# Kernel optimization log

Measured on AMD Instinct MI355X. Metric: run time of the kernel, lower is better.

The kernel has to match this reference:

```python
import jax, jax.numpy as jnp
import numpy as np
from jax import lax

# Quantized ConvBnA block: int8 conv with int32 accumulation, per-channel
# bias add (folded BN), power-of-two requant via arithmetic right shift,
# clamp, and narrow-int cast (uint8 since Act_min >= 0 -> pure_positive).

N, CIN, COUT, H, W, K = 32, 128, 256, 56, 56, 3

def setup_inputs() -> dict:
    key = jax.random.key(0)
    k1, k2, k3 = jax.random.split(key, 3)
    # int8-valued inputs / weights (stored as int32 per harness dtype support)
    x = jax.random.randint(k1, (N, CIN, H, W), -64, 64, dtype=jnp.int32)
    weight = jax.random.randint(k2, (COUT, CIN, K, K), -128, 128, dtype=jnp.int32)
    # BN_shift is negative (shift right by -n = 8 bits)
    n = jnp.full((1, COUT, 1, 1), -8, dtype=jnp.int32)
    # folded-BN integer bias, broadcasts over [N, C, H, W]
    t = jax.random.randint(k3, (1, COUT, 1, 1), -2048, 2048, dtype=jnp.int32)
    act_min = 0
    act_max = 255
    return {"x": x, "weight": weight, "n": n, "t": t,
            "act_min": act_min, "act_max": act_max}

def reference(x, weight, n, t, act_min, act_max):
    # int32-accumulated convolution (stride 1, pad 1, dilation 1, groups 1)
    acc = lax.conv_general_dilated(
        x.astype(jnp.int32), weight.astype(jnp.int32),
        window_strides=(1, 1), padding=((1, 1), (1, 1)),
        dimension_numbers=("NCHW", "OIHW", "NCHW"))
    acc = acc + t                              # folded-BN bias add
    acc = jnp.right_shift(acc, -n)             # pow2 requant, arithmetic shift
    acc = jnp.clip(acc, jnp.int32(act_min), jnp.int32(act_max))
    # pure_positive (Act_min >= 0) -> small unsigned type
    return acc.astype(jnp.uint8)
```

## Files before the change

kernel.cpp:

```cpp
#include <hip/hip_runtime.h>
#include <cstdint>


typedef __attribute__((ext_vector_type(4))) int i32x4;
typedef __attribute__((ext_vector_type(2))) int i32x2;

#define C_IN   128
#define HW2    3136
#define OUT_NSTRIDE 802816

#define XQ_BYTES 12845056
#define WQ_OFF   XQ_BYTES
#define WQ_BYTES 294912
#define ZP_OFF   (WQ_OFF + WQ_BYTES)

__device__ __forceinline__ void gload_lds16(const void* g, void* l) {
  __builtin_amdgcn_global_load_lds(
      (const __attribute__((address_space(1))) void*)(uintptr_t)g,
      (__attribute__((address_space(3))) void*)(uint32_t)(uintptr_t)l,
      16, 0, 0);
}

__global__ __launch_bounds__(256) void prep(const int* __restrict__ x,
                                            const int* __restrict__ w,
                                            char* __restrict__ xq,
                                            char* __restrict__ wq,
                                            int* __restrict__ zp) {
  int bid = blockIdx.x;
  if (bid >= 1568) {
    int id = (bid - 1568) * 256 + threadIdx.x;
    int ci = id & 127;
    int co = (id >> 7) & 255;
    int g  = id >> 15;
    wq[id] = (char)w[co * 1152 + ci * 9 + g];
    if (bid == 1568 && threadIdx.x < 64) zp[threadIdx.x] = 0;
    return;
  }
  int hb = bid % 49;
  int n  = bid / 49;
  int t  = threadIdx.x;
  int cig = t & 15;
  int hw0 = (t >> 4) * 4;
  const int* src = x + n * (C_IN * HW2) + hb * 64 + hw0;
  i32x4 ld[8];
#pragma unroll
  for (int j = 0; j < 8; j++)
    ld[j] = *(const i32x4*)(src + (cig * 8 + j) * HW2);
  char* dst = xq + (size_t)(n * HW2 + hb * 64 + hw0) * 128 + cig * 8;
#pragma unroll
  for (int p = 0; p < 4; p++) {
    unsigned lo = (ld[0][p] & 255) | ((ld[1][p] & 255) << 8) |
                  ((ld[2][p] & 255) << 16) | ((unsigned)(ld[3][p] & 255) << 24);
    unsigned hi = (ld[4][p] & 255) | ((ld[5][p] & 255) << 8) |
                  ((ld[6][p] & 255) << 16) | ((unsigned)(ld[7][p] & 255) << 24);
    i32x2 v; v[0] = (int)lo; v[1] = (int)hi;
    *(i32x2*)(dst + p * 128) = v;
  }
}

__global__ __launch_bounds__(256, 2) void conv_mfma(
    const char* __restrict__ xq, const char* __restrict__ wq,
    const char* __restrict__ zp,
    const int* __restrict__ nshift, const int* __restrict__ tbias,
    const int* __restrict__ aminp, const int* __restrict__ amaxp,
    int* __restrict__ out) {
  __shared__ char lds[65536];

  const int tid = threadIdx.x;
  const int bid = blockIdx.x;
  const int bm = bid & 1;
  const int pb = bid >> 1;
  const int l  = tid & 63;
  const int wid = tid >> 6;
  const int wm = wid >> 1, wn = wid & 1;

  const int chl = tid & 7;
  const int rsw = (tid >> 3) & 7;
  const int chg = chl ^ rsw;
  const int kboff = chg * 16;

  int p_idx[4], p_h[4], p_w[4];
#pragma unroll
  for (int i = 0; i < 4; i++) {
    int pr = (tid >> 3) + i * 32;
    int p  = pb * 128 + pr;
    int n  = p / HW2;
    int hw = p - n * HW2;
    int h  = hw / 56;
    int w  = hw - h * 56;
    p_idx[i] = p; p_h[i] = h; p_w[i] = w;
  }

  auto stageAB = [&](int g, int buf) {
    char* Ab = lds + buf * 32768;
    char* Bb = Ab + 16384;
    const int dh = g / 3 - 1, dw = g % 3 - 1;
    const int doff = dh * 56 + dw;
    const char* wsrc = wq + (((g * 256 + bm * 128)) << 7) + kboff;
#pragma unroll
    for (int i = 0; i < 4; i++) {
      int row = (tid >> 3) + i * 32;
      gload_lds16(wsrc + (row << 7), Ab + (tid + i * 256) * 16);
    }
#pragma unroll
    for (int i = 0; i < 4; i++) {
      int h2 = p_h[i] + dh, w2 = p_w[i] + dw;
      bool valid = ((unsigned)h2 < 56u) && ((unsigned)w2 < 56u);
      const char* gp = valid ? (xq + ((size_t)(p_idx[i] + doff) << 7) + kboff)
                             : zp;
      gload_lds16(gp, Bb + (tid + i * 256) * 16);
    }
  };

  i32x4 acc[4][4] = {};
  const int lrow = l & 15;
  const int lk   = (l >> 4) * 16;
  const int lsw  = (l & 7) << 4;

  auto computeStep = [&](int buf) {
    char* Ab = lds + buf * 32768;
    char* Bb = Ab + 16384;
#pragma unroll
    for (int kk = 0; kk < 2; kk++) {
      i32x4 a[4], b[4];
      const int cb = ((kk * 64 + lk) ^ lsw);
#pragma unroll
      for (int mi = 0; mi < 4; mi++) {
        int row = wm * 64 + mi * 16 + lrow;
        a[mi] = *(const i32x4*)(Ab + (row << 7) + cb);
      }
#pragma unroll
      for (int ni = 0; ni < 4; ni++) {
        int row = wn * 64 + ni * 16 + lrow;
        b[ni] = *(const i32x4*)(Bb + (row << 7) + cb);
      }
#pragma unroll
      for (int mi = 0; mi < 4; mi++)
#pragma unroll
        for (int ni = 0; ni < 4; ni++)
          acc[mi][ni] = __builtin_amdgcn_mfma_i32_16x16x64_i8(
              a[mi], b[ni], acc[mi][ni], 0, 0, 0);
    }
  };

  stageAB(0, 0);
#pragma unroll 1
  for (int s = 0; s < 9; ++s) {
    const int s1 = s + 1;
    if (s1 < 9) stageAB(s1, s1 & 1);
    __builtin_amdgcn_sched_barrier(0);
    if (s1 < 9) { asm volatile("s_waitcnt vmcnt(8)" ::: "memory"); }
    else        { asm volatile("s_waitcnt vmcnt(0)" ::: "memory"); }
    __builtin_amdgcn_s_barrier();
    __builtin_amdgcn_sched_barrier(0);
    computeStep(s & 1);
    __builtin_amdgcn_sched_barrier(0);
    __builtin_amdgcn_s_barrier();
    __builtin_amdgcn_sched_barrier(0);
  }

  const int amin = aminp[0], amax = amaxp[0];
  int pbase[4];
#pragma unroll
  for (int ni = 0; ni < 4; ni++) {
    int pp = pb * 128 + wn * 64 + ni * 16 + lrow;
    int nn = pp / HW2;
    int hh = pp - nn * HW2;
    pbase[ni] = nn * OUT_NSTRIDE + hh;
  }
#pragma unroll
  for (int mi = 0; mi < 4; mi++) {
    int co0 = bm * 128 + wm * 64 + mi * 16 + ((l >> 4) << 2);
    const int4 t4 = *(const int4*)(tbias + co0);
    const int4 n4 = *(const int4*)(nshift + co0);
#pragma unroll
    for (int ni = 0; ni < 4; ni++) {
#pragma unroll
      for (int r = 0; r < 4; r++) {
        int tv = (r == 0) ? t4.x : (r == 1) ? t4.y : (r == 2) ? t4.z : t4.w;
        int nv = (r == 0) ? n4.x : (r == 1) ? n4.y : (r == 2) ? n4.z : n4.w;
        int v = acc[mi][ni][r] + tv;
        v = v >> (-nv);
        v = v < amin ? amin : (v > amax ? amax : v);
        out[pbase[ni] + (co0 + r) * HW2] = v;
      }
    }
  }
}

extern "C" void kernel_launch(void* const* d_in, const int* in_sizes, int n_in,
                              void* d_out, int out_size, void* d_ws, size_t ws_size,
                              hipStream_t stream) {
  const int* x      = (const int*)d_in[0];
  const int* w      = (const int*)d_in[1];
  const int* nshift = (const int*)d_in[2];
  const int* tbias  = (const int*)d_in[3];
  const int* aminp  = (const int*)d_in[4];
  const int* amaxp  = (const int*)d_in[5];
  int* out = (int*)d_out;

  char* xq = (char*)d_ws;
  char* wq = (char*)d_ws + WQ_OFF;
  char* zp = (char*)d_ws + ZP_OFF;

  hipLaunchKernelGGL(prep, dim3(2720), dim3(256), 0, stream, x, w, xq, wq, (int*)zp);
  hipLaunchKernelGGL(conv_mfma, dim3(1568), dim3(256), 0, stream,
                     xq, wq, zp, nshift, tbias, aminp, amaxp, out);
}
```

Baseline: 182.5 us.

## Load weight fragments directly into registers and stage only activations in LDS

Weight tiles no longer go through LDS: each wave reads its A fragments straight from global memory into registers at the start of every filter tap. Only the shifted activation tiles remain double-buffered in LDS, which halves the shared-memory footprint and removes the A-side LDS writes and reads. The wait count is lowered to match the smaller number of outstanding staging loads. MFMA sections are also wrapped in s_setprio to favour waves that are issuing matrix ops. The trade-off is that weight loads are neither prefetched nor shared across waves, so their global or L2 latency sits on the critical path each step and sibling waves read the same data twice.

```diff
diff --git a/kernel.cpp b/kernel.cpp
--- a/kernel.cpp
+++ b/kernel.cpp
@@ -64,7 +64,7 @@
     const int* __restrict__ nshift, const int* __restrict__ tbias,
     const int* __restrict__ aminp, const int* __restrict__ amaxp,
     int* __restrict__ out) {
-  __shared__ char lds[65536];
+  __shared__ char lds[32768];
 
   const int tid = threadIdx.x;
   const int bid = blockIdx.x;
@@ -91,17 +91,10 @@
     p_idx[i] = p; p_h[i] = h; p_w[i] = w;
   }
 
-  auto stageAB = [&](int g, int buf) {
-    char* Ab = lds + buf * 32768;
-    char* Bb = Ab + 16384;
+  auto stageB = [&](int g, int buf) {
+    char* Bb = lds + buf * 16384;
     const int dh = g / 3 - 1, dw = g % 3 - 1;
     const int doff = dh * 56 + dw;
-    const char* wsrc = wq + (((g * 256 + bm * 128)) << 7) + kboff;
-#pragma unroll
-    for (int i = 0; i < 4; i++) {
-      int row = (tid >> 3) + i * 32;
-      gload_lds16(wsrc + (row << 7), Ab + (tid + i * 256) * 16);
-    }
 #pragma unroll
     for (int i = 0; i < 4; i++) {
       int h2 = p_h[i] + dh, w2 = p_w[i] + dw;
@@ -117,43 +110,44 @@
   const int lk   = (l >> 4) * 16;
   const int lsw  = (l & 7) << 4;
 
-  auto computeStep = [&](int buf) {
-    char* Ab = lds + buf * 32768;
-    char* Bb = Ab + 16384;
+  const char* abase = wq + (size_t)((bm * 128 + wm * 64 + lrow) << 7) + lk;
+
+  stageB(0, 0);
+#pragma unroll 1
+  for (int s = 0; s < 9; ++s) {
+    i32x4 a2[2][4];
+    const char* ap = abase + s * 32768;
+#pragma unroll
+    for (int kk = 0; kk < 2; kk++)
+#pragma unroll
+      for (int mi = 0; mi < 4; mi++)
+        a2[kk][mi] = *(const i32x4*)(ap + mi * 2048 + kk * 64);
+    const int s1 = s + 1;
+    if (s1 < 9) stageB(s1, s1 & 1);
+    __builtin_amdgcn_sched_barrier(0);
+    if (s1 < 9) { asm volatile("s_waitcnt vmcnt(4)" ::: "memory"); }
+    else        { asm volatile("s_waitcnt vmcnt(0)" ::: "memory"); }
+    __builtin_amdgcn_s_barrier();
+    __builtin_amdgcn_sched_barrier(0);
+    char* Bb = lds + (s & 1) * 16384;
 #pragma unroll
     for (int kk = 0; kk < 2; kk++) {
-      i32x4 a[4], b[4];
+      i32x4 b[4];
       const int cb = ((kk * 64 + lk) ^ lsw);
-#pragma unroll
-      for (int mi = 0; mi < 4; mi++) {
-        int row = wm * 64 + mi * 16 + lrow;
-        a[mi] = *(const i32x4*)(Ab + (row << 7) + cb);
-      }
 #pragma unroll
       for (int ni = 0; ni < 4; ni++) {
         int row = wn * 64 + ni * 16 + lrow;
         b[ni] = *(const i32x4*)(Bb + (row << 7) + cb);
       }
+      __builtin_amdgcn_s_setprio(1);
 #pragma unroll
       for (int mi = 0; mi < 4; mi++)
 #pragma unroll
         for (int ni = 0; ni < 4; ni++)
           acc[mi][ni] = __builtin_amdgcn_mfma_i32_16x16x64_i8(
-              a[mi], b[ni], acc[mi][ni], 0, 0, 0);
+              a2[kk][mi], b[ni], acc[mi][ni], 0, 0, 0);
+      __builtin_amdgcn_s_setprio(0);
     }
-  };
-
-  stageAB(0, 0);
-#pragma unroll 1
-  for (int s = 0; s < 9; ++s) {
-    const int s1 = s + 1;
-    if (s1 < 9) stageAB(s1, s1 & 1);
-    __builtin_amdgcn_sched_barrier(0);
-    if (s1 < 9) { asm volatile("s_waitcnt vmcnt(8)" ::: "memory"); }
-    else        { asm volatile("s_waitcnt vmcnt(0)" ::: "memory"); }
-    __builtin_amdgcn_s_barrier();
-    __builtin_amdgcn_sched_barrier(0);
-    computeStep(s & 1);
     __builtin_amdgcn_sched_barrier(0);
     __builtin_amdgcn_s_barrier();
     __builtin_amdgcn_sched_barrier(0);
```

Measured after the change: 217.2 us. 19.0% more time.
